# Kernel optimization log

Measured on AMD Instinct MI355X. Metric: run time of the kernel, lower is better.

## Reference

```python
import jax, jax.numpy as jnp
import numpy as np

N_NODES = 50000
N_EDGES = 800000
D = 128          # input_node_dim == output_node_dim (residual)
T = 3            # number of node types == number of edge types
NODE_IN = D + T * D  # node updater input dim = 512


def setup_inputs() -> dict:
    key = jax.random.key(0)
    ks = jax.random.split(key, 8)
    scale = 0.05
    return {
        "node_feature": jax.random.normal(ks[0], (N_NODES, D), jnp.float32),
        "W_e": jax.random.normal(ks[1], (T, D, D), jnp.float32) * scale,
        "b_e": jnp.zeros((T, D), jnp.float32),
        "W_n": jax.random.normal(ks[2], (T, D, NODE_IN), jnp.float32) * scale,
        "b_n": jnp.zeros((T, D), jnp.float32),
        "edge_src": jax.random.randint(ks[3], (N_EDGES,), 0, N_NODES, jnp.int32),
        "edge_dst": jax.random.randint(ks[4], (N_EDGES,), 0, N_NODES, jnp.int32),
        "edge_type": jax.random.randint(ks[5], (N_EDGES,), 0, T, jnp.int32),
        "node_type": jax.random.randint(ks[6], (N_NODES,), 0, T, jnp.int32),
    }


def reference(node_feature, W_e, b_e, W_n, b_n, edge_src, edge_dst, edge_type, node_type):
    N, Din = node_feature.shape
    n_types = W_e.shape[0]
    out_dim = W_e.shape[1]

    # message_function: per-edge-type MLP on source features, relu, zero elsewhere
    src = node_feature[edge_src]                      # [E, D] gather
    parts = [jax.nn.relu(node_feature)]               # reduce_function relu's node_feature
    for t in range(n_types):
        msg = jax.nn.relu(src @ W_e[t].T + b_e[t])    # [E, out]
        msg = jnp.where((edge_type == t)[:, None], msg, jnp.zeros((), msg.dtype))
        # mailbox sum over incoming edges per destination node
        parts.append(jax.ops.segment_sum(msg, edge_dst, num_segments=N))
    agg = jnp.concatenate(parts, axis=1)              # [N, D + T*out]

    # per-node-type updater MLP, dispatched by node_type
    updated = jnp.zeros((N, out_dim), node_feature.dtype)
    for t in range(n_types):
        o = agg @ W_n[t].T + b_n[t]                   # [N, out]
        updated = jnp.where((node_type == t)[:, None], o, updated)

    # use_residual = True
    return updated + node_feature
```

## Files before the change

kernel.cpp:

```cpp
#include <hip/hip_runtime.h>
#include <hip/hip_bf16.h>

#define NN 50000
#define NE 800000
#define DD 128
#define NT 3
#define AGGW 384
#define EM 64
#define EM2 128
#define LDK 136
#define CB 32
#define LDK2 520
#define NBITS 7
#define NBINS ((NN + 127) / 128)
#define EPB 2048
#define BINCAP 2560
#define NTILES_MAX (((NN + EM - 1) / EM) + NT)
#define NTILE_PAD (((NTILES_MAX + 7) / 8) * 8)

typedef __bf16 bf16x8 __attribute__((ext_vector_type(8)));
typedef float f32x4 __attribute__((ext_vector_type(4)));
typedef unsigned short u16x8 __attribute__((ext_vector_type(8)));

__device__ __forceinline__ unsigned short f2b(float f) {
    __hip_bfloat16 h = __float2bfloat16(f);
    return __builtin_bit_cast(unsigned short, h);
}
__device__ __forceinline__ float b2f(unsigned int u16bits) {
    unsigned int x = u16bits << 16;
    return __builtin_bit_cast(float, x);
}

__global__ void k_zero(int* __restrict__ bhist, int* __restrict__ cnts) {
    int i = blockIdx.x * blockDim.x + threadIdx.x;
    if (i < NBINS) bhist[i] = 0;
    if (i >= NBINS && i < NBINS + 16) cnts[i - NBINS] = 0;
}

__global__ void k_prep(const float* __restrict__ nf, const float* __restrict__ We,
                       const float* __restrict__ Wn, unsigned short* __restrict__ nfb,
                       unsigned short* __restrict__ Web, unsigned short* __restrict__ Wnb) {
    const size_t n0 = (size_t)NN * DD / 8;
    const size_t n1 = (size_t)NT * DD * DD / 8;
    const size_t n2 = (size_t)NT * DD * 512 / 8;
    size_t i = (size_t)blockIdx.x * blockDim.x + threadIdx.x;
    size_t total = n0 + n1 + n2;
    for (size_t p = i; p < total; p += (size_t)gridDim.x * blockDim.x) {
        const float* s; unsigned short* d; size_t off;
        if (p < n0)            { s = nf; d = nfb; off = p; }
        else if (p < n0 + n1)  { s = We; d = Web; off = p - n0; }
        else                   { s = Wn; d = Wnb; off = p - n0 - n1; }
        const float4* f4 = (const float4*)(s + off * 8);
        float4 x = f4[0], y = f4[1];
        u16x8 u = { f2b(x.x), f2b(x.y), f2b(x.z), f2b(x.w),
                    f2b(y.x), f2b(y.y), f2b(y.z), f2b(y.w) };
        *(u16x8*)(d + off * 8) = u;
    }
}

__global__ __launch_bounds__(256) void k_binhist(const int* __restrict__ edst,
        const int* __restrict__ ntp, int* __restrict__ bhist, int* __restrict__ cnts) {
    __shared__ int lh[NBINS];
    __shared__ int ln[3];
    int tid = threadIdx.x;
    for (int i = tid; i < NBINS; i += 256) lh[i] = 0;
    if (tid < 3) ln[tid] = 0;
    __syncthreads();
    int i0 = blockIdx.x * blockDim.x + tid;
    int stride = gridDim.x * blockDim.x;
    for (int p = i0; p < NE; p += stride) atomicAdd(&lh[edst[p] >> NBITS], 1);
    for (int p = i0; p < NN; p += stride) atomicAdd(&ln[ntp[p]], 1);
    __syncthreads();
    for (int i = tid; i < NBINS; i += 256) if (lh[i]) atomicAdd(&bhist[i], lh[i]);
    if (tid < 3) atomicAdd(&cnts[6 + tid], ln[tid]);
}

__global__ __launch_bounds__(512) void k_binscan(const int* __restrict__ bhist,
        int* __restrict__ binptr, int* __restrict__ bincur, int* __restrict__ rowptr) {
    __shared__ int sa[NBINS], sb[NBINS];
    int tid = threadIdx.x;
    if (tid < NBINS) sa[tid] = bhist[tid];
    __syncthreads();
    int flip = 0;
    for (int off = 1; off < NBINS; off <<= 1) {
        int* src = flip ? sb : sa;
        int* dst = flip ? sa : sb;
        if (tid < NBINS) dst[tid] = src[tid] + ((tid >= off) ? src[tid - off] : 0);
        __syncthreads();
        flip ^= 1;
    }
    int* inc = flip ? sb : sa;
    if (tid < NBINS) {
        int excl = (tid == 0) ? 0 : inc[tid - 1];
        binptr[tid] = excl;
        bincur[tid] = excl;
    }
    if (tid == 0) { binptr[NBINS] = NE; rowptr[NN] = NE; }
}

__global__ __launch_bounds__(256) void k_binscatter(const int* __restrict__ esrc,
        const int* __restrict__ edst, const int* __restrict__ et,
        const int* __restrict__ ntp, int* __restrict__ bincur, int* __restrict__ cnts,
        int* __restrict__ pe, int* __restrict__ sn) {
    const int NEB = (NE + EPB - 1) / EPB;
    __shared__ int lh[NBINS], gb[NBINS], lr[NBINS];
    __shared__ int lcnt[3], lbase[3];
    int tid = threadIdx.x, b = blockIdx.x;
    if (b < NEB) {
        for (int i = tid; i < NBINS; i += 256) { lh[i] = 0; lr[i] = 0; }
        __syncthreads();
        int e0 = b * EPB;
        for (int i = 0; i < EPB; i += 256) {
            int e = e0 + i + tid;
            if (e < NE) atomicAdd(&lh[edst[e] >> NBITS], 1);
        }
        __syncthreads();
        for (int i = tid; i < NBINS; i += 256)
            if (lh[i]) gb[i] = atomicAdd(&bincur[i], lh[i]);
        __syncthreads();
        for (int i = 0; i < EPB; i += 256) {
            int e = e0 + i + tid;
            if (e < NE) {
                int d = edst[e];
                int t = et[e];
                int bin = d >> NBITS;
                int rank = atomicAdd(&lr[bin], 1);
                pe[gb[bin] + rank] = (t * NN + esrc[e]) | ((d & 127) << 18) | (t << 25);
            }
        }
    } else {
        if (tid < 3) lcnt[tid] = 0;
        __syncthreads();
        int p = (b - NEB) * 256 + tid;
        int t = -1, rank = 0;
        if (p < NN) { t = ntp[p]; rank = atomicAdd(&lcnt[t], 1); }
        __syncthreads();
        if (tid < 3) lbase[tid] = atomicAdd(&cnts[9 + tid], lcnt[tid]);
        __syncthreads();
        if (p < NN) {
            int c0 = cnts[6], c1 = cnts[7];
            int off = (t == 0) ? 0 : (t == 1) ? c0 : c0 + c1;
            sn[off + lbase[t] + rank] = p;
        }
    }
}

__global__ __launch_bounds__(256) void k_binsort(const int* __restrict__ binptr,
        int* __restrict__ pe, int* __restrict__ rowptr) {
    __shared__ int lcnt[128], lrk[128], lrp[128];
    __shared__ unsigned int sorted[BINCAP];
    int b = blockIdx.x, tid = threadIdx.x;
    int beg = binptr[b], end = binptr[b + 1];
    int cnt = min(end - beg, BINCAP);
    if (tid < 128) { lcnt[tid] = 0; lrk[tid] = 0; }
    __syncthreads();
    for (int e = tid; e < cnt; e += 256)
        atomicAdd(&lcnt[(pe[beg + e] >> 18) & 127], 1);
    __syncthreads();
    if (tid < 64) {
        int v = lcnt[2 * tid] + lcnt[2 * tid + 1];
        int s = v;
        for (int d = 1; d < 64; d <<= 1) {
            int u = __shfl_up(s, d);
            if (tid >= d) s += u;
        }
        int excl = s - v;
        lrp[2 * tid] = excl;
        lrp[2 * tid + 1] = excl + lcnt[2 * tid];
    }
    __syncthreads();
    if (tid < 128) {
        int node = b * 128 + tid;
        if (node < NN) rowptr[node] = beg + lrp[tid];
    }
    for (int e = tid; e < cnt; e += 256) {
        unsigned int p = pe[beg + e];
        int d = (p >> 18) & 127;
        int pos = lrp[d] + atomicAdd(&lrk[d], 1);
        sorted[pos] = p;
    }
    __syncthreads();
    for (int e = tid; e < cnt; e += 256) pe[beg + e] = sorted[e];
}

__global__ __launch_bounds__(512, 4) void k_msg(const unsigned short* __restrict__ nfb,
        const unsigned short* __restrict__ Web, const float* __restrict__ be,
        unsigned short* __restrict__ M) {
    __shared__ unsigned short Wsm[DD][LDK];
    const int TILES = (NN + EM2 - 1) / EM2;
    int b = blockIdx.x;
    int t = b / TILES, tile = b % TILES;
    int base = tile * EM2;
    int m = min(EM2, NN - base);
    int tid = threadIdx.x;
    {
        int row = tid >> 2, c0 = (tid & 3) * 32;
        const u16x8* src = (const u16x8*)(Web + ((size_t)t * DD + row) * DD + c0);
#pragma unroll
        for (int v = 0; v < 4; ++v) *(u16x8*)&Wsm[row][c0 + v * 8] = src[v];
    }
    __syncthreads();

    int wave = tid >> 6, l = tid & 63, lr = l & 15, kg = l >> 4;
    int arow = min(base + wave * 16 + lr, NN - 1);
    const u16x8* Arow = (const u16x8*)(nfb + (size_t)arow * DD);
    f32x4 acc[8];
#pragma unroll
    for (int n = 0; n < 8; n++) acc[n] = (f32x4){0.f, 0.f, 0.f, 0.f};
#pragma unroll
    for (int k0 = 0; k0 < DD; k0 += 32) {
        bf16x8 a = __builtin_bit_cast(bf16x8, Arow[(k0 >> 3) + kg]);
#pragma unroll
        for (int n = 0; n < 8; n++) {
            bf16x8 bb = *(const bf16x8*)&Wsm[n * 16 + lr][k0 + kg * 8];
            acc[n] = __builtin_amdgcn_mfma_f32_16x16x32_bf16(a, bb, acc[n], 0, 0, 0);
        }
    }
    unsigned short* Mt = M + (size_t)t * NN * DD;
#pragma unroll
    for (int n = 0; n < 8; n++) {
        int col = n * 16 + lr;
        float bias = be[t * DD + col];
#pragma unroll
        for (int r = 0; r < 4; r++) {
            int row = wave * 16 + kg * 4 + r;
            if (row < m) {
                float v = acc[n][r] + bias;
                Mt[(size_t)(base + row) * DD + col] = f2b(fmaxf(v, 0.f));
            }
        }
    }
}

__global__ __launch_bounds__(256) void k_agg(const unsigned short* __restrict__ M,
        const int* __restrict__ rowptr, const int* __restrict__ pe,
        unsigned short* __restrict__ aggb) {
    int wid = blockIdx.x * 4 + (threadIdx.x >> 6);
    int l = threadIdx.x & 63;
    if (wid >= NN) return;
    int beg = rowptr[wid], end = rowptr[wid + 1];
    const unsigned int* Mu = (const unsigned int*)M;
    float a0x = 0.f, a0y = 0.f, a1x = 0.f, a1y = 0.f, a2x = 0.f, a2y = 0.f;
    int e = beg;
    for (; e + 16 <= end; e += 16) {
        unsigned int p[16], v[16];
#pragma unroll
        for (int j = 0; j < 16; ++j) p[j] = pe[e + j];
#pragma unroll
        for (int j = 0; j < 16; ++j) v[j] = Mu[((p[j] & 0x3FFFFu) << 6) | l];
#pragma unroll
        for (int j = 0; j < 16; ++j) {
            int t = p[j] >> 25;
            float lo = __builtin_bit_cast(float, v[j] << 16);
            float hi = __builtin_bit_cast(float, v[j] & 0xFFFF0000u);
            if (t == 0) { a0x += lo; a0y += hi; }
            else if (t == 1) { a1x += lo; a1y += hi; }
            else { a2x += lo; a2y += hi; }
        }
    }
    while (e < end) {
        unsigned int p[8], v[8];
#pragma unroll
        for (int j = 0; j < 8; ++j) p[j] = pe[min(e + j, end - 1)];
#pragma unroll
        for (int j = 0; j < 8; ++j) v[j] = Mu[((p[j] & 0x3FFFFu) << 6) | l];
#pragma unroll
        for (int j = 0; j < 8; ++j) {
            if (e + j < end) {
                int t = p[j] >> 25;
                float lo = __builtin_bit_cast(float, v[j] << 16);
                float hi = __builtin_bit_cast(float, v[j] & 0xFFFF0000u);
                if (t == 0) { a0x += lo; a0y += hi; }
                else if (t == 1) { a1x += lo; a1y += hi; }
                else { a2x += lo; a2y += hi; }
            }
        }
        e += 8;
    }
    unsigned int* dst = (unsigned int*)(aggb + (size_t)wid * AGGW);
    dst[l]       = (unsigned int)f2b(a0x) | ((unsigned int)f2b(a0y) << 16);
    dst[64 + l]  = (unsigned int)f2b(a1x) | ((unsigned int)f2b(a1y) << 16);
    dst[128 + l] = (unsigned int)f2b(a2x) | ((unsigned int)f2b(a2y) << 16);
}

__global__ __launch_bounds__(256, 3) void k_node(const float* __restrict__ nf,
        const unsigned short* __restrict__ nfb, const unsigned short* __restrict__ Wnb,
        const float* __restrict__ bn, const int* __restrict__ sn,
        const int* __restrict__ cnts, const unsigned short* __restrict__ aggb,
        float* __restrict__ out) {
    __shared__ unsigned short Wsm[CB][LDK2];
    int c0 = cnts[6], c1 = cnts[7], c2 = cnts[8];
    int n0 = (c0 + EM - 1) / EM, n1 = (c1 + EM - 1) / EM, n2 = (c2 + EM - 1) / EM;
    int ntile = n0 + n1 + n2;
    int b = blockIdx.x;
    int rt = (b & 7) * (NTILE_PAD / 8) + (b >> 3);
    if (rt >= ntile) return;
    int tid = threadIdx.x;
    int wave = tid >> 6, l = tid & 63, lr = l & 15, kg = l >> 4;
    int t, tile;
    if (rt < n0) { t = 0; tile = rt; }
    else if (rt < n0 + n1) { t = 1; tile = rt - n0; }
    else { t = 2; tile = rt - n0 - n1; }
    int off = (t == 0) ? 0 : (t == 1) ? c0 : c0 + c1;
    int cntt = (t == 0) ? c0 : (t == 1) ? c1 : c2;
    int base = off + tile * EM;
    int m = min(EM, cntt - tile * EM);

    int myrow = sn[base + min(wave * 16 + lr, m - 1)];
    const u16x8* An = (const u16x8*)(nfb + (size_t)myrow * DD);
    const u16x8* Ag = (const u16x8*)(aggb + (size_t)myrow * AGGW);
    u16x8 afr[16];
#pragma unroll
    for (int kc = 0; kc < 4; ++kc) {
#pragma unroll
        for (int k0 = 0; k0 < DD; k0 += 32) {
            u16x8 araw;
            if (kc == 0) {
                araw = An[(k0 >> 3) + kg];
#pragma unroll
                for (int j = 0; j < 8; ++j)
                    araw[j] = (araw[j] & 0x8000) ? (unsigned short)0 : araw[j];
            } else {
                araw = Ag[((kc - 1) * DD + k0) / 8 + kg];
            }
            afr[kc * 4 + (k0 >> 5)] = araw;
        }
    }

    int nd[4];
#pragma unroll
    for (int r = 0; r < 4; ++r) nd[r] = sn[base + min(wave * 16 + kg * 4 + r, m - 1)];

    int srow = tid & 31, scc = (tid >> 5) * 64;
#pragma unroll 1
    for (int cbk = 0; cbk < 4; ++cbk) {
        if (cbk) __syncthreads();
        const u16x8* src = (const u16x8*)(Wnb + ((size_t)t * DD + cbk * CB + srow) * 512 + scc);
#pragma unroll
        for (int v = 0; v < 8; ++v) *(u16x8*)&Wsm[srow][scc + v * 8] = src[v];
        __syncthreads();

        f32x4 acc0 = {0.f, 0.f, 0.f, 0.f}, acc1 = {0.f, 0.f, 0.f, 0.f};
#pragma unroll
        for (int kc = 0; kc < 4; ++kc) {
#pragma unroll
            for (int k0 = 0; k0 < DD; k0 += 32) {
                bf16x8 a = __builtin_bit_cast(bf16x8, afr[kc * 4 + (k0 >> 5)]);
                int kw = kc * DD + k0 + kg * 8;
                bf16x8 b0 = *(const bf16x8*)&Wsm[lr][kw];
                bf16x8 b1 = *(const bf16x8*)&Wsm[16 + lr][kw];
                acc0 = __builtin_amdgcn_mfma_f32_16x16x32_bf16(a, b0, acc0, 0, 0, 0);
                acc1 = __builtin_amdgcn_mfma_f32_16x16x32_bf16(a, b1, acc1, 0, 0, 0);
            }
        }
#pragma unroll
        for (int n = 0; n < 2; n++) {
            int col = cbk * CB + n * 16 + lr;
            float bias = bn[t * DD + col];
            const f32x4& av = n ? acc1 : acc0;
#pragma unroll
            for (int r = 0; r < 4; r++) {
                int row = wave * 16 + kg * 4 + r;
                if (row < m) {
                    int node = nd[r];
                    out[(size_t)node * DD + col] = av[r] + bias + nf[(size_t)node * DD + col];
                }
            }
        }
    }
}

extern "C" void kernel_launch(void* const* d_in, const int* in_sizes, int n_in,
                              void* d_out, int out_size, void* d_ws, size_t ws_size,
                              hipStream_t stream) {
    const float* nf   = (const float*)d_in[0];
    const float* We   = (const float*)d_in[1];
    const float* be   = (const float*)d_in[2];
    const float* Wn   = (const float*)d_in[3];
    const float* bn   = (const float*)d_in[4];
    const int*   esrc = (const int*)d_in[5];
    const int*   edst = (const int*)d_in[6];
    const int*   et   = (const int*)d_in[7];
    const int*   ntp  = (const int*)d_in[8];
    float* out = (float*)d_out;

    char* w = (char*)d_ws;
    unsigned short* M    = (unsigned short*)w;  w += (size_t)NT * NN * DD * 2;
    unsigned short* aggb = (unsigned short*)w;  w += (size_t)NN * AGGW * 2;
    unsigned short* nfb  = (unsigned short*)w;  w += (size_t)NN * DD * 2;
    unsigned short* Web  = (unsigned short*)w;  w += (size_t)NT * DD * DD * 2;
    unsigned short* Wnb  = (unsigned short*)w;  w += (size_t)NT * DD * 512 * 2;
    int* pe     = (int*)w;  w += (size_t)NE * 4;
    int* bhist  = (int*)w;  w += (NBINS + 1) * 4;
    int* binptr = (int*)w;  w += (NBINS + 1) * 4;
    int* bincur = (int*)w;  w += (NBINS + 1) * 4;
    int* rowptr = (int*)w;  w += (size_t)(NN + 1) * 4;
    int* sn     = (int*)w;  w += (size_t)NN * 4;
    int* cnts   = (int*)w;  w += 16 * 4;

    const int NEB = (NE + EPB - 1) / EPB;
    const int NCH = (NN + 255) / 256;
    const int TILES2 = (NN + EM2 - 1) / EM2;

    k_zero<<<2, 256, 0, stream>>>(bhist, cnts);
    k_prep<<<1024, 256, 0, stream>>>(nf, We, Wn, nfb, Web, Wnb);
    k_binhist<<<256, 256, 0, stream>>>(edst, ntp, bhist, cnts);
    k_binscan<<<1, 512, 0, stream>>>(bhist, binptr, bincur, rowptr);
    k_binscatter<<<NEB + NCH, 256, 0, stream>>>(esrc, edst, et, ntp, bincur, cnts, pe, sn);
    k_binsort<<<NBINS, 256, 0, stream>>>(binptr, pe, rowptr);
    k_msg<<<NT * TILES2, 512, 0, stream>>>(nfb, Web, be, M);
    k_agg<<<(NN + 3) / 4, 256, 0, stream>>>(M, rowptr, pe, aggb);
    k_node<<<NTILE_PAD, 256, 0, stream>>>(nf, nfb, Wnb, bn, sn, cnts, aggb, out);
}
```

Before: 151.0 us.

## Use 16 lanes per node with 128-bit loads in edge aggregation

Each destination node is now handled by 16 threads instead of a full 64-lane wave. Each thread loads a uint4 (8 bf16 values) per edge message rather than one 32-bit word, and stores its outputs as 128-bit writes. This packs four nodes into each wave and cuts the number of load instructions, which aims to hide latency and reduce wasted lanes on low-degree nodes. In exchange it uses more accumulator registers, drops the 16-wide unrolled fast path, and relies on NN being divisible by 16 since the bounds check was removed.

```diff
diff --git a/kernel.cpp b/kernel.cpp
--- a/kernel.cpp
+++ b/kernel.cpp
@@ -235,52 +235,60 @@
 __global__ __launch_bounds__(256) void k_agg(const unsigned short* __restrict__ M,
         const int* __restrict__ rowptr, const int* __restrict__ pe,
         unsigned short* __restrict__ aggb) {
-    int wid = blockIdx.x * 4 + (threadIdx.x >> 6);
-    int l = threadIdx.x & 63;
-    if (wid >= NN) return;
-    int beg = rowptr[wid], end = rowptr[wid + 1];
-    const unsigned int* Mu = (const unsigned int*)M;
-    float a0x = 0.f, a0y = 0.f, a1x = 0.f, a1y = 0.f, a2x = 0.f, a2y = 0.f;
+    int node = blockIdx.x * 16 + (threadIdx.x >> 4);
+    int q = threadIdx.x & 15;
+    int beg = rowptr[node], end = rowptr[node + 1];
+    const uint4* Mu4 = (const uint4*)M;
+    float a0[8] = {0,0,0,0,0,0,0,0};
+    float a1[8] = {0,0,0,0,0,0,0,0};
+    float a2[8] = {0,0,0,0,0,0,0,0};
     int e = beg;
-    for (; e + 16 <= end; e += 16) {
-        unsigned int p[16], v[16];
-#pragma unroll
-        for (int j = 0; j < 16; ++j) p[j] = pe[e + j];
-#pragma unroll
-        for (int j = 0; j < 16; ++j) v[j] = Mu[((p[j] & 0x3FFFFu) << 6) | l];
-#pragma unroll
-        for (int j = 0; j < 16; ++j) {
-            int t = p[j] >> 25;
-            float lo = __builtin_bit_cast(float, v[j] << 16);
-            float hi = __builtin_bit_cast(float, v[j] & 0xFFFF0000u);
-            if (t == 0) { a0x += lo; a0y += hi; }
-            else if (t == 1) { a1x += lo; a1y += hi; }
-            else { a2x += lo; a2y += hi; }
-        }
-    }
     while (e < end) {
-        unsigned int p[8], v[8];
+        unsigned int p[8];
+        uint4 v[8];
 #pragma unroll
         for (int j = 0; j < 8; ++j) p[j] = pe[min(e + j, end - 1)];
 #pragma unroll
-        for (int j = 0; j < 8; ++j) v[j] = Mu[((p[j] & 0x3FFFFu) << 6) | l];
+        for (int j = 0; j < 8; ++j)
+            if (e + j < end) v[j] = Mu4[(size_t)(p[j] & 0x3FFFFu) * 16 + q];
 #pragma unroll
         for (int j = 0; j < 8; ++j) {
             if (e + j < end) {
                 int t = p[j] >> 25;
-                float lo = __builtin_bit_cast(float, v[j] << 16);
-                float hi = __builtin_bit_cast(float, v[j] & 0xFFFF0000u);
-                if (t == 0) { a0x += lo; a0y += hi; }
-                else if (t == 1) { a1x += lo; a1y += hi; }
-                else { a2x += lo; a2y += hi; }
+                float f0 = b2f(v[j].x & 0xFFFF), f1 = b2f(v[j].x >> 16);
+                float f2 = b2f(v[j].y & 0xFFFF), f3 = b2f(v[j].y >> 16);
+                float f4 = b2f(v[j].z & 0xFFFF), f5 = b2f(v[j].z >> 16);
+                float f6 = b2f(v[j].w & 0xFFFF), f7 = b2f(v[j].w >> 16);
+                if (t == 0) {
+                    a0[0] += f0; a0[1] += f1; a0[2] += f2; a0[3] += f3;
+                    a0[4] += f4; a0[5] += f5; a0[6] += f6; a0[7] += f7;
+                } else if (t == 1) {
+                    a1[0] += f0; a1[1] += f1; a1[2] += f2; a1[3] += f3;
+                    a1[4] += f4; a1[5] += f5; a1[6] += f6; a1[7] += f7;
+                } else {
+                    a2[0] += f0; a2[1] += f1; a2[2] += f2; a2[3] += f3;
+                    a2[4] += f4; a2[5] += f5; a2[6] += f6; a2[7] += f7;
+                }
             }
         }
         e += 8;
     }
-    unsigned int* dst = (unsigned int*)(aggb + (size_t)wid * AGGW);
-    dst[l]       = (unsigned int)f2b(a0x) | ((unsigned int)f2b(a0y) << 16);
-    dst[64 + l]  = (unsigned int)f2b(a1x) | ((unsigned int)f2b(a1y) << 16);
-    dst[128 + l] = (unsigned int)f2b(a2x) | ((unsigned int)f2b(a2y) << 16);
+    unsigned int* dst = (unsigned int*)(aggb + (size_t)node * AGGW);
+    uint4 o0 = { (unsigned int)f2b(a0[0]) | ((unsigned int)f2b(a0[1]) << 16),
+                 (unsigned int)f2b(a0[2]) | ((unsigned int)f2b(a0[3]) << 16),
+                 (unsigned int)f2b(a0[4]) | ((unsigned int)f2b(a0[5]) << 16),
+                 (unsigned int)f2b(a0[6]) | ((unsigned int)f2b(a0[7]) << 16) };
+    uint4 o1 = { (unsigned int)f2b(a1[0]) | ((unsigned int)f2b(a1[1]) << 16),
+                 (unsigned int)f2b(a1[2]) | ((unsigned int)f2b(a1[3]) << 16),
+                 (unsigned int)f2b(a1[4]) | ((unsigned int)f2b(a1[5]) << 16),
+                 (unsigned int)f2b(a1[6]) | ((unsigned int)f2b(a1[7]) << 16) };
+    uint4 o2 = { (unsigned int)f2b(a2[0]) | ((unsigned int)f2b(a2[1]) << 16),
+                 (unsigned int)f2b(a2[2]) | ((unsigned int)f2b(a2[3]) << 16),
+                 (unsigned int)f2b(a2[4]) | ((unsigned int)f2b(a2[5]) << 16),
+                 (unsigned int)f2b(a2[6]) | ((unsigned int)f2b(a2[7]) << 16) };
+    ((uint4*)dst)[q]        = o0;
+    ((uint4*)(dst + 64))[q] = o1;
+    ((uint4*)(dst + 128))[q] = o2;
 }
 
 __global__ __launch_bounds__(256, 3) void k_node(const float* __restrict__ nf,
@@ -409,6 +417,6 @@
     k_binscatter<<<NEB + NCH, 256, 0, stream>>>(esrc, edst, et, ntp, bincur, cnts, pe, sn);
     k_binsort<<<NBINS, 256, 0, stream>>>(binptr, pe, rowptr);
     k_msg<<<NT * TILES2, 512, 0, stream>>>(nfb, Web, be, M);
-    k_agg<<<(NN + 3) / 4, 256, 0, stream>>>(M, rowptr, pe, aggb);
+    k_agg<<<NN / 16, 256, 0, stream>>>(M, rowptr, pe, aggb);
     k_node<<<NTILE_PAD, 256, 0, stream>>>(nf, nfb, Wnb, bn, sn, cnts, aggb, out);
 }
```

Result: no change. 153.1 us (+1.4%).
